# Optimization experiments

Measured on AMD Instinct MI355X. Metric: run time of the kernel, lower is better.

The kernel has to match this reference:

```python
import jax, jax.numpy as jnp
import numpy as np

N, E, L = 20000, 320000, 12
DH, DE, DHE, DRES = 64, 8, 16, 16
SC_F, BB_F = 21, 12
EPS = 1e-5
LETTERS = 'ARNDCQEGHILKMFPSTWYV'
_G = {'A':[0,0,0,0],'R':[1,1,1,1],'N':[1,1,0,0],'D':[1,1,0,0],'C':[1,0,0,0],'Q':[1,1,1,0],'E':[1,1,1,0],'G':[0,0,0,0],'H':[1,1,0,0],'I':[1,1,0,0],'L':[1,1,0,0],'K':[1,1,1,1],'M':[1,1,1,0],'F':[1,1,0,0],'P':[0,0,0,0],'S':[1,0,0,0],'T':[1,0,0,0],'W':[1,1,0,0],'Y':[1,1,0,0],'V':[1,0,0,0]}
CHI_TABLE = jnp.asarray(np.array([_G[a] for a in LETTERS], dtype=np.float32))  # [20,4]


def bn(x, g, b):
    # BatchNorm1d in inference mode with running_mean=0, running_var=1
    return x / jnp.sqrt(1.0 + EPS) * g + b


def gat(x, src, dst, Wl, Wr, att, Wres, bias, edge=None, We=None):
    # single-head GATv2Conv (PyG semantics: messages src->dst, residual projection)
    n = x.shape[0]
    xl = x @ Wl                       # [N,DH]
    m = xl[src] + (x @ Wr)[dst]       # [E,DH] gather
    if edge is not None:
        m = m + edge @ We
    e = jax.nn.leaky_relu(m, 0.2) @ att               # [E]
    emax = jax.ops.segment_max(e, dst, num_segments=n)
    ex = jnp.exp(e - emax[dst])
    den = jax.ops.segment_sum(ex, dst, num_segments=n)
    alpha = ex / (den[dst] + 1e-16)                   # segment softmax over incoming edges
    out = jax.ops.segment_sum(alpha[:, None] * xl[src], dst, num_segments=n)
    return out + bias + x @ Wres


def setup_inputs() -> dict:
    key = jax.random.key(0)
    ks = iter(jax.random.split(key, 80))
    def nrm(*s):
        return jax.random.normal(next(ks), s, jnp.float32) * 0.05
    inp = {}
    inp['sidechain_node_features'] = jax.random.normal(next(ks), (N, SC_F), jnp.float32)
    inp['backbone_node_features'] = jax.random.normal(next(ks), (N, BB_F), jnp.float32)
    inp['sidechain_edge_attrs'] = jax.random.normal(next(ks), (E, DE), jnp.float32)
    inp['sidechain_edges'] = jax.random.randint(next(ks), (2, E), 0, N)
    inp['backbone_edges'] = jax.random.randint(next(ks), (2, E), 0, N)
    inp['residue_ids'] = jax.random.randint(next(ks), (N,), 0, 20)
    inp['sc_emb_W'] = nrm(SC_F, DH); inp['sc_emb_b'] = nrm(DH)
    inp['bb_emb_W'] = nrm(BB_F, DH); inp['bb_emb_b'] = nrm(DH)
    inp['res_table'] = nrm(20, DRES)
    inp['rr_W1'] = nrm(2 * DRES, DHE); inp['rr_b1'] = nrm(DHE)
    inp['rr_W2'] = nrm(DHE, 1); inp['rr_b2'] = nrm(1)
    inp['sc_Wl'] = nrm(L, DH, DH); inp['sc_Wr'] = nrm(L, DH, DH)
    inp['sc_We'] = nrm(L, DE, DH); inp['sc_att'] = nrm(L, DH)
    inp['sc_res'] = nrm(L, DH, DH); inp['sc_bias'] = nrm(L, DH)
    inp['bb_Wl'] = nrm(L, DH, DH); inp['bb_Wr'] = nrm(L, DH, DH)
    inp['bb_att'] = nrm(L, DH); inp['bb_res'] = nrm(L, DH, DH); inp['bb_bias'] = nrm(L, DH)
    inp['eu_W1'] = nrm(L, DE, DHE); inp['eu_b1'] = nrm(L, DHE)
    inp['eu_g'] = jnp.ones((L, DHE)); inp['eu_beta'] = jnp.zeros((L, DHE))
    inp['eu_W2'] = nrm(L, DHE, DE); inp['eu_b2'] = nrm(L, DE)
    inp['bnu_W'] = nrm(DH, DH); inp['bnu_b'] = nrm(DH)
    inp['bnu_g'] = jnp.ones((DH,)); inp['bnu_beta'] = jnp.zeros((DH,))
    inp['af_W'] = nrm(DH, 1); inp['af_b'] = nrm(1)
    inp['af_g'] = jnp.ones((1,)); inp['af_beta'] = jnp.zeros((1,))
    inp['chi_W'] = nrm(4, DH, DH); inp['chi_b'] = nrm(4, DH)
    inp['ad_W1'] = nrm(DH, DH); inp['ad_W2'] = nrm(DH, 1)
    inp['vc_W1'] = nrm(DH, DH); inp['vc_b1'] = nrm(DH)
    inp['vc_W2'] = nrm(DH, 3); inp['vc_b2'] = nrm(3)
    inp['bbh_W1'] = nrm(4, DH, DH); inp['bbh_b1'] = nrm(4, DH)
    inp['phi_W2'] = nrm(DH, 1); inp['psi_W2'] = nrm(DH, 1)
    inp['xca_W2'] = nrm(DH, 3); inp['xca_b2'] = nrm(3)
    inp['vcb_W2'] = nrm(DH, 3); inp['vcb_b2'] = nrm(3)
    return inp


def reference(sidechain_node_features, backbone_node_features, sidechain_edge_attrs, sidechain_edges, backbone_edges, residue_ids, sc_emb_W, sc_emb_b, bb_emb_W, bb_emb_b, res_table, rr_W1, rr_b1, rr_W2, rr_b2, sc_Wl, sc_Wr, sc_We, sc_att, sc_res, sc_bias, bb_Wl, bb_Wr, bb_att, bb_res, bb_bias, eu_W1, eu_b1, eu_g, eu_beta, eu_W2, eu_b2, bnu_W, bnu_b, bnu_g, bnu_beta, af_W, af_b, af_g, af_beta, chi_W, chi_b, ad_W1, ad_W2, vc_W1, vc_b1, vc_W2, vc_b2, bbh_W1, bbh_b1, phi_W2, psi_W2, xca_W2, xca_b2, vcb_W2, vcb_b2):
    # node embeddings (dropout = identity in eval)
    sc = jax.nn.relu(sidechain_node_features @ sc_emb_W + sc_emb_b)
    bb = jax.nn.relu(backbone_node_features @ bb_emb_W + bb_emb_b)
    # residue-relation gating of sidechain edge attrs
    re = res_table[residue_ids]                      # [N,DRES]
    src, dst = sidechain_edges[0], sidechain_edges[1]
    cat = jnp.concatenate([re[src], re[dst]], axis=-1)
    rel = jax.nn.sigmoid(jax.nn.relu(cat @ rr_W1 + rr_b1) @ rr_W2 + rr_b2)  # [E,1]
    ea = sidechain_edge_attrs * rel
    bsrc, bdst = backbone_edges[0], backbone_edges[1]
    for l in range(L):
        # EdgeUpdate: Linear-BN-ReLU-Linear + residual
        h = jax.nn.relu(bn(ea @ eu_W1[l] + eu_b1[l], eu_g[l], eu_beta[l]))
        ea = h @ eu_W2[l] + eu_b2[l] + ea
        sc = gat(sc, src, dst, sc_Wl[l], sc_Wr[l], sc_att[l], sc_res[l], sc_bias[l], ea, sc_We[l])
        bb = gat(bb, bsrc, bdst, bb_Wl[l], bb_Wr[l], bb_att[l], bb_res[l], bb_bias[l])
    # AttentionFusion gates BackboneNodeUpdate(sc) into bb
    sc_up = jax.nn.relu(bn(sc @ bnu_W + bnu_b, bnu_g, bnu_beta))
    attn = jax.nn.sigmoid(bn(sc @ af_W + af_b, af_g, af_beta))
    bb = bb + attn * sc_up
    # sidechain heads with chi masks
    mask = CHI_TABLE[residue_ids]                    # [N,4]
    chis = []
    for i in range(4):
        h = jax.nn.relu(sc @ chi_W[i] + chi_b[i]) * mask[:, i:i + 1]
        chis.append(jax.nn.relu(h @ ad_W1) @ ad_W2)
    v_com = jax.nn.relu(sc @ vc_W1 + vc_b1) @ vc_W2 + vc_b2
    # backbone heads
    phi = jax.nn.relu(bb @ bbh_W1[0] + bbh_b1[0]) @ phi_W2
    psi = jax.nn.relu(bb @ bbh_W1[1] + bbh_b1[1]) @ psi_W2
    X_c_alpha = jax.nn.relu(bb @ bbh_W1[2] + bbh_b1[2]) @ xca_W2 + xca_b2
    V_c_beta = jax.nn.relu(bb @ bbh_W1[3] + bbh_b1[3]) @ vcb_W2 + vcb_b2
    return (chis[0], chis[1], chis[2], chis[3], v_com, phi, psi, X_c_alpha, V_c_beta)
```

## Files before the change

kernel.cpp:

```cpp
#include <hip/hip_runtime.h>
#include <hip/hip_bf16.h>

#define NN 20000
#define NE 320000
#define NL 12
#define BN_C 0.9999950000374997f


#define CHI_PACK ( (0ull<<0)|(4ull<<3)|(2ull<<6)|(2ull<<9)|(1ull<<12)|(3ull<<15)|(3ull<<18)|(0ull<<21) \
                 | (2ull<<24)|(2ull<<27)|(2ull<<30)|(4ull<<33)|(3ull<<36)|(2ull<<39)|(0ull<<42)|(1ull<<45) \
                 | (1ull<<48)|(2ull<<51)|(2ull<<54)|(1ull<<57) )
__device__ __forceinline__ float chi_mask(int res, int i){
  int nchi = (int)((CHI_PACK >> (3*res)) & 7ull);
  return (i < nchi) ? 1.f : 0.f;
}

__device__ __forceinline__ float wsum(float v){
  #pragma unroll
  for (int off = 32; off > 0; off >>= 1) v += __shfl_xor(v, off);
  return v;
}
__device__ __forceinline__ float leaky(float x){
  return fmaxf(x, 0.f) + 0.2f*fminf(x, 0.f);
}

__global__ __launch_bounds__(256) void k_init(int* p, int n){
  int i = blockIdx.x*256 + threadIdx.x;
  if (i < n) p[i] = 0;
}

__global__ __launch_bounds__(256) void k_mark(float* out){
  int i = blockIdx.x*256 + threadIdx.x;
  if (i < NN) out[i] = 9.0f;
}

__global__ __launch_bounds__(256) void k_pre(
    const float* __restrict__ Xsc, const float* __restrict__ Xbb,
    const float* __restrict__ Wsc, const float* __restrict__ bsc,
    const float* __restrict__ Wbb, const float* __restrict__ bbb,
    const int* __restrict__ scE, const int* __restrict__ bbE,
    float* __restrict__ sc, float* __restrict__ bbuf, int* cnt_sc, int* cnt_bb){
  int b = blockIdx.x, t = threadIdx.x;
  if (b < 5000){
    int tid = b*256 + t;
    int node = tid >> 6, d = tid & 63;
    float acc = bsc[d];
    #pragma unroll
    for (int k = 0; k < 21; k++) acc += Xsc[node*21+k] * Wsc[k*64+d];
    sc[tid] = fmaxf(acc, 0.f);
  } else if (b < 10000){
    int tid = (b-5000)*256 + t;
    int node = tid >> 6, d = tid & 63;
    float acc = bbb[d];
    #pragma unroll
    for (int k = 0; k < 12; k++) acc += Xbb[node*12+k] * Wbb[k*64+d];
    bbuf[tid] = fmaxf(acc, 0.f);
  } else if (b < 11250){
    int e = (b-10000)*256 + t;
    atomicAdd(&cnt_sc[scE[NE + e]], 1);
  } else {
    int e = (b-11250)*256 + t;
    atomicAdd(&cnt_bb[bbE[NE + e]], 1);
  }
}

__global__ __launch_bounds__(256) void k_scan(
    int* cnt_sc, int* cnt_bb, int* rp_sc, int* rp_bb,
    const float* __restrict__ resT, const float* __restrict__ rrW1,
    const float* __restrict__ rrb1, const float* __restrict__ rrW2,
    const float* __restrict__ rrb2, float* relTab){
  int t = threadIdx.x;
  if (blockIdx.x == 2){
    __shared__ float sRT[320], sW1[512], sB1[16], sW2[16];
    for (int i = t; i < 320; i += 256) sRT[i] = resT[i];
    for (int i = t; i < 512; i += 256) sW1[i] = rrW1[i];
    if (t < 16){ sB1[t] = rrb1[t]; sW2[t] = rrW2[t]; }
    __syncthreads();
    float b2v = rrb2[0];
    for (int p = t; p < 400; p += 256){
      int a = p / 20, c = p % 20;
      const float* ra = &sRT[a*16];
      const float* rc = &sRT[c*16];
      float z = b2v;
      #pragma unroll
      for (int j = 0; j < 16; j++){
        float h = sB1[j];
        #pragma unroll
        for (int i = 0; i < 16; i++) h += ra[i] * sW1[i*16+j];
        #pragma unroll
        for (int i = 0; i < 16; i++) h += rc[i] * sW1[(16+i)*16+j];
        z += fmaxf(h, 0.f) * sW2[j];
      }
      relTab[p] = 1.f / (1.f + __expf(-z));
    }
    return;
  }
  int* cnt = blockIdx.x ? cnt_bb : cnt_sc;
  int* rp  = blockIdx.x ? rp_bb  : rp_sc;
  __shared__ int s[256];
  const int CH = 79;
  int beg = t * CH;
  int sum = 0;
  for (int i = beg; i < beg + CH && i < NN; i++) sum += cnt[i];
  s[t] = sum; __syncthreads();
  for (int off = 1; off < 256; off <<= 1){
    int v = (t >= off) ? s[t-off] : 0;
    __syncthreads();
    s[t] += v;
    __syncthreads();
  }
  int run = (t == 0) ? 0 : s[t-1];
  for (int i = beg; i < beg + CH && i < NN; i++){
    int c = cnt[i];
    rp[i] = run;
    cnt[i] = run;
    run += c;
  }
  if (t == 0) rp[NN] = NE;
}

__global__ __launch_bounds__(256) void k_scatter(
    const int* __restrict__ scE, const int* __restrict__ bbE, const int* __restrict__ rid,
    const float* __restrict__ relTab, const float* __restrict__ attrs,
    int* cur_sc, int* cur_bb, int* __restrict__ ps_sc, int* __restrict__ ps_bb,
    float* __restrict__ ea){
  int b = blockIdx.x, t = threadIdx.x;
  if (b < 1250){
    int e = b*256 + t;
    int s = scE[e], d = scE[NE + e];
    float rel = relTab[rid[s]*20 + rid[d]];
    float4 A = ((const float4*)attrs)[e*2];
    float4 B = ((const float4*)attrs)[e*2+1];
    A.x *= rel; A.y *= rel; A.z *= rel; A.w *= rel;
    B.x *= rel; B.y *= rel; B.z *= rel; B.w *= rel;
    int pos = atomicAdd(&cur_sc[d], 1);
    ps_sc[pos] = s;
    ((float4*)ea)[pos*2]   = A;
    ((float4*)ea)[pos*2+1] = B;
  } else {
    int e = (b-1250)*256 + t;
    int s = bbE[e], d = bbE[NE + e];
    int pos = atomicAdd(&cur_bb[d], 1);
    ps_bb[pos] = s;
  }
}

__device__ void node_mm(float* sx, const float* __restrict__ x,
                        const float* __restrict__ Wl, const float* __restrict__ Wr,
                        const float* __restrict__ Wres, const float* __restrict__ bias, int l,
                        float* __restrict__ xl, float* __restrict__ xr, float* __restrict__ base,
                        int tile){
  int t = threadIdx.x;
  for (int i = t; i < 1024; i += 256) sx[i] = x[tile*1024 + i];
  __syncthreads();
  int d = t & 63, r = t >> 6;
  int wo = l*4096 + d;
  float aL[4] = {0,0,0,0}, aR[4] = {0,0,0,0}, aB[4];
  float bv = bias[l*64 + d];
  #pragma unroll
  for (int j = 0; j < 4; j++) aB[j] = bv;
  #pragma unroll 4
  for (int k = 0; k < 64; k++){
    float wl = Wl[wo + k*64], wr = Wr[wo + k*64], ws = Wres[wo + k*64];
    #pragma unroll
    for (int j = 0; j < 4; j++){
      float xv = sx[(r + 4*j)*64 + k];
      aL[j] += xv*wl; aR[j] += xv*wr; aB[j] += xv*ws;
    }
  }
  int n0 = tile*16 + r;
  #pragma unroll
  for (int j = 0; j < 4; j++){
    int n = n0 + 4*j;
    xl[n*64+d] = aL[j]; xr[n*64+d] = aR[j]; base[n*64+d] = aB[j];
  }
}

__global__ __launch_bounds__(256) void k_layer1(
    float* __restrict__ ea, int l,
    const float* __restrict__ euW1, const float* __restrict__ eub1,
    const float* __restrict__ eug, const float* __restrict__ eube,
    const float* __restrict__ euW2, const float* __restrict__ eub2,
    const float* __restrict__ sc, const float* __restrict__ bbv,
    const float* __restrict__ scWl, const float* __restrict__ scWr,
    const float* __restrict__ scRes, const float* __restrict__ scBias,
    const float* __restrict__ bbWl, const float* __restrict__ bbWr,
    const float* __restrict__ bbRes, const float* __restrict__ bbBias,
    float* __restrict__ xl_sc, float* __restrict__ xr_sc, float* __restrict__ bs_sc,
    float* __restrict__ xl_bb, float* __restrict__ xr_bb, float* __restrict__ bs_bb){
  __shared__ float smem[1024];
  int b = blockIdx.x, t = threadIdx.x;
  if (b < 1250){
    float* sW1 = smem;        float* sB1 = smem+128; float* sG  = smem+144;
    float* sBe = smem+160;    float* sW2 = smem+176; float* sB2 = smem+304;
    for (int i = t; i < 128; i += 256){ sW1[i] = euW1[l*128+i]; sW2[i] = euW2[l*128+i]; }
    if (t < 16){ sB1[t] = eub1[l*16+t]; sG[t] = eug[l*16+t]; sBe[t] = eube[l*16+t]; }
    if (t < 8) sB2[t] = eub2[l*8+t];
    __syncthreads();
    int e = b*256 + t;
    float4 A = ((const float4*)ea)[e*2];
    float4 B = ((const float4*)ea)[e*2+1];
    float a[8] = {A.x,A.y,A.z,A.w,B.x,B.y,B.z,B.w};
    float h[16];
    #pragma unroll
    for (int j = 0; j < 16; j++){
      float v = sB1[j];
      #pragma unroll
      for (int i = 0; i < 8; i++) v += a[i] * sW1[i*16+j];
      h[j] = fmaxf(v*BN_C*sG[j] + sBe[j], 0.f);
    }
    #pragma unroll
    for (int i = 0; i < 8; i++){
      float v = sB2[i] + a[i];
      #pragma unroll
      for (int j = 0; j < 16; j++) v += h[j] * sW2[j*8+i];
      a[i] = v;
    }
    ((float4*)ea)[e*2]   = make_float4(a[0],a[1],a[2],a[3]);
    ((float4*)ea)[e*2+1] = make_float4(a[4],a[5],a[6],a[7]);
  } else if (b < 2500){
    node_mm(smem, sc, scWl, scWr, scRes, scBias, l, xl_sc, xr_sc, bs_sc, b-1250);
  } else {
    node_mm(smem, bbv, bbWl, bbWr, bbRes, bbBias, l, xl_bb, xr_bb, bs_bb, b-2500);
  }
}

__global__ __launch_bounds__(256) void k_agg(
    float* __restrict__ sc, float* __restrict__ bbv, int l,
    const float* __restrict__ xl_sc, const float* __restrict__ xr_sc, const float* __restrict__ bs_sc,
    const float* __restrict__ xl_bb, const float* __restrict__ xr_bb, const float* __restrict__ bs_bb,
    const int* __restrict__ rp_sc, const int* __restrict__ ps_sc,
    const int* __restrict__ rp_bb, const int* __restrict__ ps_bb,
    const float* __restrict__ ea, const float* __restrict__ We,
    const float* __restrict__ scAtt, const float* __restrict__ bbAtt){
  int b = blockIdx.x;
  int lane = threadIdx.x & 63, wid = threadIdx.x >> 6;
  int half = lane >> 5, l2 = lane & 31;
  bool is_sc = b < 5000;
  int n = (is_sc ? b : b - 5000)*4 + wid;
  const float* xl = is_sc ? xl_sc : xl_bb;
  const float* xr = is_sc ? xr_sc : xr_bb;
  const float* bs = is_sc ? bs_sc : bs_bb;
  const int* rp = is_sc ? rp_sc : rp_bb;
  const int* ps = is_sc ? ps_sc : ps_bb;
  const float2* xl2 = (const float2*)xl;
  float2 att2 = ((const float2*)((is_sc ? scAtt : bbAtt) + l*64))[l2];
  float2 w[8];
  if (is_sc){
    #pragma unroll
    for (int j = 0; j < 8; j++) w[j] = ((const float2*)(We + l*512 + j*64))[l2];
  }
  int beg = rp[n], end = rp[n+1];
  float2 xr2 = ((const float2*)xr)[n*32 + l2];
  float ox = 0.f, oy = 0.f, s = 0.f;
  if (beg < end){
    int last = end - 1;
    int ia = min(beg + half, last);
    int ib = min(beg + 2 + half, last);
    float2 vA = xl2[ps[ia]*32 + l2];
    float2 vB = xl2[ps[ib]*32 + l2];
    for (int eid = beg; eid < end; eid += 4){
      int nx = eid + 4;
      int ia_n = min(nx + half, last);
      int ib_n = min(nx + 2 + half, last);
      float2 vA_n = xl2[ps[ia_n]*32 + l2];
      float2 vB_n = xl2[ps[ib_n]*32 + l2];
      bool va = eid + half < end;
      bool vb = eid + 2 + half < end;
      float mAx = vA.x + xr2.x, mAy = vA.y + xr2.y;
      float mBx = vB.x + xr2.x, mBy = vB.y + xr2.y;
      if (is_sc){
        int cia = min(eid + half, last);
        int cib = min(eid + 2 + half, last);
        const float4* pa4 = (const float4*)(ea + (size_t)cia*8);
        float4 A = pa4[0], B = pa4[1];
        float av[8] = {A.x,A.y,A.z,A.w,B.x,B.y,B.z,B.w};
        #pragma unroll
        for (int j = 0; j < 8; j++){ mAx += av[j]*w[j].x; mAy += av[j]*w[j].y; }
        const float4* pb4 = (const float4*)(ea + (size_t)cib*8);
        A = pb4[0]; B = pb4[1];
        float bvv[8] = {A.x,A.y,A.z,A.w,B.x,B.y,B.z,B.w};
        #pragma unroll
        for (int j = 0; j < 8; j++){ mBx += bvv[j]*w[j].x; mBy += bvv[j]*w[j].y; }
      }
      float eA = leaky(mAx)*att2.x + leaky(mAy)*att2.y;
      float eB = leaky(mBx)*att2.x + leaky(mBy)*att2.y;
      #pragma unroll
      for (int off = 1; off <= 16; off <<= 1){
        eA += __shfl_xor(eA, off);
        eB += __shfl_xor(eB, off);
      }
      float pA = va ? __expf(eA) : 0.f;
      float pB = vb ? __expf(eB) : 0.f;
      ox += pA*vA.x + pB*vB.x;
      oy += pA*vA.y + pB*vB.y;
      s  += pA + pB;
      vA = vA_n; vB = vB_n;
    }
  }
  ox += __shfl_xor(ox, 32);
  oy += __shfl_xor(oy, 32);
  s  += __shfl_xor(s, 32);
  if (half == 0){
    float2 bsv = ((const float2*)bs)[n*32 + l2];
    float inv = 1.f/(s + 1e-16f);
    float2 r;
    r.x = ox*inv + bsv.x;
    r.y = oy*inv + bsv.y;
    ((float2*)(is_sc ? sc : bbv))[n*32 + l2] = r;
  }
}

__global__ __launch_bounds__(256) void k_heads(
    const float* __restrict__ sc, const float* __restrict__ bbv, const int* __restrict__ rid,
    const float* __restrict__ bnuW, const float* __restrict__ bnub,
    const float* __restrict__ bnug, const float* __restrict__ bnube,
    const float* __restrict__ afW, const float* __restrict__ afb,
    const float* __restrict__ afg, const float* __restrict__ afbe,
    const float* __restrict__ vcW1, const float* __restrict__ vcb1,
    const float* __restrict__ vcW2, const float* __restrict__ vcb2,
    const float* __restrict__ chiW, const float* __restrict__ chib,
    const float* __restrict__ adW1, const float* __restrict__ adW2,
    const float* __restrict__ bbhW1, const float* __restrict__ bbhb1,
    const float* __restrict__ phiW2, const float* __restrict__ psiW2,
    const float* __restrict__ xcaW2, const float* __restrict__ xcab2,
    const float* __restrict__ vcbW2, const float* __restrict__ vcbb2,
    float* __restrict__ out){
  __shared__ float sx[1024];
  __shared__ float sh[1024];
  __shared__ int srid[16];
  int b = blockIdx.x, t = threadIdx.x;
  int d = t & 63, r = t >> 6;
  if (b < 1250){
    int tile = b;
    for (int i = t; i < 1024; i += 256) sx[i] = sc[tile*1024 + i];
    if (t < 16) srid[t] = rid[tile*16 + t];
    __syncthreads();
    for (int i = 0; i < 4; i++){
      const float* W = chiW + i*4096;
      float acc[4] = {0,0,0,0};
      #pragma unroll 4
      for (int k = 0; k < 64; k++){
        float w = W[k*64+d];
        #pragma unroll
        for (int j = 0; j < 4; j++) acc[j] += sx[(r + 4*j)*64 + k] * w;
      }
      float bi = chib[i*64+d];
      #pragma unroll
      for (int j = 0; j < 4; j++){
        float mk = chi_mask(srid[r + 4*j], i);
        sh[(r + 4*j)*64 + d] = fmaxf(acc[j] + bi, 0.f) * mk;
      }
      __syncthreads();
      float a2[4] = {0,0,0,0};
      #pragma unroll 4
      for (int k = 0; k < 64; k++){
        float w = adW1[k*64+d];
        #pragma unroll
        for (int j = 0; j < 4; j++) a2[j] += sh[(r + 4*j)*64 + k] * w;
      }
      float w2 = adW2[d];
      #pragma unroll
      for (int j = 0; j < 4; j++){
        float p = wsum(fmaxf(a2[j], 0.f) * w2);
        if (d == 0) out[i*NN + tile*16 + r + 4*j] = p;
      }
      __syncthreads();
    }
  } else {
    int tile = b - 1250;
    for (int i = t; i < 1024; i += 256){ sx[i] = sc[tile*1024 + i]; sh[i] = bbv[tile*1024 + i]; }
    __syncthreads();
    float aU[4] = {0,0,0,0}, aV[4] = {0,0,0,0};
    #pragma unroll 4
    for (int k = 0; k < 64; k++){
      float wu = bnuW[k*64+d], wv = vcW1[k*64+d];
      #pragma unroll
      for (int j = 0; j < 4; j++){
        float xv = sx[(r + 4*j)*64 + k];
        aU[j] += xv*wu; aV[j] += xv*wv;
      }
    }
    float afwd = afW[d];
    float bnubd = bnub[d], bnugd = bnug[d], bnubed = bnube[d];
    float vcb1d = vcb1[d];
    float afbv = afb[0], afgv = afg[0], afbev = afbe[0];
    #pragma unroll
    for (int j = 0; j < 4; j++){
      int node = tile*16 + r + 4*j;
      float z = wsum(sx[(r + 4*j)*64 + d] * afwd);
      float attn = 1.f / (1.f + __expf(-((z + afbv)*BN_C*afgv + afbev)));
      float u = fmaxf((aU[j] + bnubd)*BN_C*bnugd + bnubed, 0.f);
      sh[(r + 4*j)*64 + d] += attn*u;
      float vh = fmaxf(aV[j] + vcb1d, 0.f);
      #pragma unroll
      for (int c = 0; c < 3; c++){
        float p = wsum(vh * vcW2[d*3+c]);
        if (d == 0) out[4*NN + node*3 + c] = p + vcb2[c];
      }
    }
    __syncthreads();
    for (int i = 0; i < 4; i++){
      const float* W = bbhW1 + i*4096;
      float acc[4] = {0,0,0,0};
      #pragma unroll 4
      for (int k = 0; k < 64; k++){
        float w = W[k*64+d];
        #pragma unroll
        for (int j = 0; j < 4; j++) acc[j] += sh[(r + 4*j)*64 + k] * w;
      }
      float bi = bbhb1[i*64+d];
      if (i < 2){
        float w2 = (i == 0) ? phiW2[d] : psiW2[d];
        #pragma unroll
        for (int j = 0; j < 4; j++){
          float p = wsum(fmaxf(acc[j] + bi, 0.f) * w2);
          if (d == 0) out[(7+i)*NN + tile*16 + r + 4*j] = p;
        }
      } else {
        const float* W2 = (i == 2) ? xcaW2 : vcbW2;
        const float* B2 = (i == 2) ? xcab2 : vcbb2;
        int off = (i == 2) ? 9*NN : 12*NN;
        #pragma unroll
        for (int j = 0; j < 4; j++){
          float h = fmaxf(acc[j] + bi, 0.f);
          #pragma unroll
          for (int c = 0; c < 3; c++){
            float p = wsum(h * W2[d*3+c]);
            if (d == 0) out[off + (tile*16 + r + 4*j)*3 + c] = p + B2[c];
          }
        }
      }
    }
  }
}

extern "C" __attribute__((visibility("default")))
void kernel_launch(void* const* d_in, const int* in_sizes, int n_in,
                   void* d_out, int out_size, void* d_ws, size_t ws_size,
                   hipStream_t stream) {
  (void)hipGetLastError();

  const float* Xsc   = (const float*)d_in[0];
  const float* Xbb   = (const float*)d_in[1];
  const float* attrs = (const float*)d_in[2];
  const int*  scE   = (const int*)d_in[3];
  const int*  bbE   = (const int*)d_in[4];
  const int*  rid   = (const int*)d_in[5];
  const float* scembW=(const float*)d_in[6];  const float* scembb=(const float*)d_in[7];
  const float* bbembW=(const float*)d_in[8];  const float* bbembb=(const float*)d_in[9];
  const float* resT  =(const float*)d_in[10];
  const float* rrW1  =(const float*)d_in[11]; const float* rrb1  =(const float*)d_in[12];
  const float* rrW2  =(const float*)d_in[13]; const float* rrb2  =(const float*)d_in[14];
  const float* scWl  =(const float*)d_in[15]; const float* scWr  =(const float*)d_in[16];
  const float* scWe  =(const float*)d_in[17]; const float* scAtt =(const float*)d_in[18];
  const float* scRes =(const float*)d_in[19]; const float* scBias=(const float*)d_in[20];
  const float* bbWl  =(const float*)d_in[21]; const float* bbWr  =(const float*)d_in[22];
  const float* bbAtt =(const float*)d_in[23]; const float* bbRes =(const float*)d_in[24];
  const float* bbBias=(const float*)d_in[25];
  const float* euW1  =(const float*)d_in[26]; const float* eub1  =(const float*)d_in[27];
  const float* eug   =(const float*)d_in[28]; const float* eube  =(const float*)d_in[29];
  const float* euW2  =(const float*)d_in[30]; const float* eub2  =(const float*)d_in[31];
  const float* bnuW  =(const float*)d_in[32]; const float* bnub  =(const float*)d_in[33];
  const float* bnug  =(const float*)d_in[34]; const float* bnube =(const float*)d_in[35];
  const float* afW   =(const float*)d_in[36]; const float* afb   =(const float*)d_in[37];
  const float* afg   =(const float*)d_in[38]; const float* afbe  =(const float*)d_in[39];
  const float* chiW  =(const float*)d_in[40]; const float* chib  =(const float*)d_in[41];
  const float* adW1  =(const float*)d_in[42]; const float* adW2  =(const float*)d_in[43];
  const float* vcW1  =(const float*)d_in[44]; const float* vcb1  =(const float*)d_in[45];
  const float* vcW2  =(const float*)d_in[46]; const float* vcb2  =(const float*)d_in[47];
  const float* bbhW1 =(const float*)d_in[48]; const float* bbhb1 =(const float*)d_in[49];
  const float* phiW2 =(const float*)d_in[50]; const float* psiW2 =(const float*)d_in[51];
  const float* xcaW2 =(const float*)d_in[52]; const float* xcab2 =(const float*)d_in[53];
  const float* vcbW2 =(const float*)d_in[54]; const float* vcbb2 =(const float*)d_in[55];
  float* out = (float*)d_out;

  size_t need = 1024 + (size_t)(8*NN*64 + NE*8)*4 + (size_t)(2*(NN+1) + 2*NN + 2*NE)*4;
  if (ws_size < need){
    k_mark<<<(NN+255)/256, 256, 0, stream>>>(out);
    return;
  }
  float* relTab = (float*)d_ws;
  float* f = (float*)((char*)d_ws + 1024);
  float* sc    = f; f += NN*64;
  float* bbuf  = f; f += NN*64;
  float* xl_sc = f; f += NN*64;
  float* xr_sc = f; f += NN*64;
  float* bs_sc = f; f += NN*64;
  float* xl_bb = f; f += NN*64;
  float* xr_bb = f; f += NN*64;
  float* bs_bb = f; f += NN*64;
  float* ea    = f; f += NE*8;
  int* ip = (int*)f;
  int* rp_sc  = ip; ip += NN+1;
  int* rp_bb  = ip; ip += NN+1;
  int* cnt_sc = ip; ip += NN;
  int* cnt_bb = ip; ip += NN;
  int* ps_sc  = ip; ip += NE;
  int* ps_bb  = ip; ip += NE;

  k_init<<<(2*NN + 255)/256, 256, 0, stream>>>(cnt_sc, 2*NN);
  k_pre<<<12500, 256, 0, stream>>>(Xsc, Xbb, scembW, scembb, bbembW, bbembb,
                                   scE, bbE, sc, bbuf, cnt_sc, cnt_bb);
  k_scan<<<3, 256, 0, stream>>>(cnt_sc, cnt_bb, rp_sc, rp_bb,
                                resT, rrW1, rrb1, rrW2, rrb2, relTab);
  k_scatter<<<2500, 256, 0, stream>>>(scE, bbE, rid, relTab, attrs,
                                      cnt_sc, cnt_bb, ps_sc, ps_bb, ea);
  for (int l = 0; l < NL; l++){
    k_layer1<<<3750, 256, 0, stream>>>(ea, l,
        euW1, eub1, eug, eube, euW2, eub2,
        sc, bbuf,
        scWl, scWr, scRes, scBias,
        bbWl, bbWr, bbRes, bbBias,
        xl_sc, xr_sc, bs_sc, xl_bb, xr_bb, bs_bb);
    k_agg<<<10000, 256, 0, stream>>>(sc, bbuf, l,
        xl_sc, xr_sc, bs_sc, xl_bb, xr_bb, bs_bb,
        rp_sc, ps_sc, rp_bb, ps_bb,
        ea, scWe, scAtt, bbAtt);
  }
  k_heads<<<2500, 256, 0, stream>>>(sc, bbuf, rid,
      bnuW, bnub, bnug, bnube, afW, afb, afg, afbe,
      vcW1, vcb1, vcW2, vcb2,
      chiW, chib, adW1, adW2, bbhW1, bbhb1,
      phiW2, psiW2, xcaW2, xcab2, vcbW2, vcbb2, out);
}
```

Baseline: 1.343 ms.

## Enlarge node matmul tiles, interleave agg blocks across XCDs, use nontemporal loads

The node projection in k_layer1 now computes 32 nodes per block instead of 16. This reuses each weight load across twice as many rows and halves the node-block count (3750 to 2500 blocks). k_agg remaps block indices so sidechain and backbone work is interleaved across the 8 XCDs, which aims at better L2 locality and load balance. Edge index and edge-attribute streams in k_agg use nontemporal loads to avoid polluting cache needed for gathered xl rows. Costs are more registers and shared memory per block and fewer blocks for latency hiding.

```diff
diff --git a/kernel.cpp b/kernel.cpp
--- a/kernel.cpp
+++ b/kernel.cpp
@@ -14,6 +14,10 @@
   int nchi = (int)((CHI_PACK >> (3*res)) & 7ull);
   return (i < nchi) ? 1.f : 0.f;
 }
+
+typedef float vf4 __attribute__((ext_vector_type(4)));
+__device__ __forceinline__ vf4 ldnt4(const float* p){ return __builtin_nontemporal_load((const vf4*)p); }
+__device__ __forceinline__ int  ldnti(const int* p){ return __builtin_nontemporal_load(p); }
 
 __device__ __forceinline__ float wsum(float v){
   #pragma unroll
@@ -145,37 +149,6 @@
   }
 }
 
-__device__ void node_mm(float* sx, const float* __restrict__ x,
-                        const float* __restrict__ Wl, const float* __restrict__ Wr,
-                        const float* __restrict__ Wres, const float* __restrict__ bias, int l,
-                        float* __restrict__ xl, float* __restrict__ xr, float* __restrict__ base,
-                        int tile){
-  int t = threadIdx.x;
-  for (int i = t; i < 1024; i += 256) sx[i] = x[tile*1024 + i];
-  __syncthreads();
-  int d = t & 63, r = t >> 6;
-  int wo = l*4096 + d;
-  float aL[4] = {0,0,0,0}, aR[4] = {0,0,0,0}, aB[4];
-  float bv = bias[l*64 + d];
-  #pragma unroll
-  for (int j = 0; j < 4; j++) aB[j] = bv;
-  #pragma unroll 4
-  for (int k = 0; k < 64; k++){
-    float wl = Wl[wo + k*64], wr = Wr[wo + k*64], ws = Wres[wo + k*64];
-    #pragma unroll
-    for (int j = 0; j < 4; j++){
-      float xv = sx[(r + 4*j)*64 + k];
-      aL[j] += xv*wl; aR[j] += xv*wr; aB[j] += xv*ws;
-    }
-  }
-  int n0 = tile*16 + r;
-  #pragma unroll
-  for (int j = 0; j < 4; j++){
-    int n = n0 + 4*j;
-    xl[n*64+d] = aL[j]; xr[n*64+d] = aR[j]; base[n*64+d] = aB[j];
-  }
-}
-
 __global__ __launch_bounds__(256) void k_layer1(
     float* __restrict__ ea, int l,
     const float* __restrict__ euW1, const float* __restrict__ eub1,
@@ -188,7 +161,7 @@
     const float* __restrict__ bbRes, const float* __restrict__ bbBias,
     float* __restrict__ xl_sc, float* __restrict__ xr_sc, float* __restrict__ bs_sc,
     float* __restrict__ xl_bb, float* __restrict__ xr_bb, float* __restrict__ bs_bb){
-  __shared__ float smem[1024];
+  __shared__ float smem[2048];
   int b = blockIdx.x, t = threadIdx.x;
   if (b < 1250){
     float* sW1 = smem;        float* sB1 = smem+128; float* sG  = smem+144;
@@ -218,10 +191,40 @@
     }
     ((float4*)ea)[e*2]   = make_float4(a[0],a[1],a[2],a[3]);
     ((float4*)ea)[e*2+1] = make_float4(a[4],a[5],a[6],a[7]);
-  } else if (b < 2500){
-    node_mm(smem, sc, scWl, scWr, scRes, scBias, l, xl_sc, xr_sc, bs_sc, b-1250);
   } else {
-    node_mm(smem, bbv, bbWl, bbWr, bbRes, bbBias, l, xl_bb, xr_bb, bs_bb, b-2500);
+    bool is_sc = b < 1875;
+    int tile = is_sc ? (b-1250) : (b-1875);
+    const float* x  = is_sc ? sc : bbv;
+    const float* Wl = is_sc ? scWl : bbWl;
+    const float* Wr = is_sc ? scWr : bbWr;
+    const float* Ws = is_sc ? scRes : bbRes;
+    const float* bias = is_sc ? scBias : bbBias;
+    float* xl = is_sc ? xl_sc : xl_bb;
+    float* xr = is_sc ? xr_sc : xr_bb;
+    float* bs = is_sc ? bs_sc : bs_bb;
+    for (int i = t; i < 2048; i += 256) smem[i] = x[tile*2048 + i];
+    __syncthreads();
+    int d = t & 63, r = t >> 6;
+    int wo = l*4096 + d;
+    float aL[8] = {0,0,0,0,0,0,0,0}, aR[8] = {0,0,0,0,0,0,0,0}, aB[8];
+    float bv = bias[l*64 + d];
+    #pragma unroll
+    for (int j = 0; j < 8; j++) aB[j] = bv;
+    #pragma unroll 2
+    for (int k = 0; k < 64; k++){
+      float wl = Wl[wo + k*64], wr = Wr[wo + k*64], ws = Ws[wo + k*64];
+      #pragma unroll
+      for (int j = 0; j < 8; j++){
+        float xv = smem[(r + 4*j)*64 + k];
+        aL[j] += xv*wl; aR[j] += xv*wr; aB[j] += xv*ws;
+      }
+    }
+    int n0 = tile*32 + r;
+    #pragma unroll
+    for (int j = 0; j < 8; j++){
+      int n = n0 + 4*j;
+      xl[n*64+d] = aL[j]; xr[n*64+d] = aR[j]; bs[n*64+d] = aB[j];
+    }
   }
 }
 
@@ -233,11 +236,12 @@
     const int* __restrict__ rp_bb, const int* __restrict__ ps_bb,
     const float* __restrict__ ea, const float* __restrict__ We,
     const float* __restrict__ scAtt, const float* __restrict__ bbAtt){
-  int b = blockIdx.x;
+  int x = blockIdx.x;
   int lane = threadIdx.x & 63, wid = threadIdx.x >> 6;
   int half = lane >> 5, l2 = lane & 31;
-  bool is_sc = b < 5000;
-  int n = (is_sc ? b : b - 5000)*4 + wid;
+  int xcd = x & 7;
+  bool is_sc = xcd < 4;
+  int n = ((x >> 3)*4 + (xcd & 3))*4 + wid;
   const float* xl = is_sc ? xl_sc : xl_bb;
   const float* xr = is_sc ? xr_sc : xr_bb;
   const float* bs = is_sc ? bs_sc : bs_bb;
@@ -257,14 +261,14 @@
     int last = end - 1;
     int ia = min(beg + half, last);
     int ib = min(beg + 2 + half, last);
-    float2 vA = xl2[ps[ia]*32 + l2];
-    float2 vB = xl2[ps[ib]*32 + l2];
+    float2 vA = xl2[ldnti(ps + ia)*32 + l2];
+    float2 vB = xl2[ldnti(ps + ib)*32 + l2];
     for (int eid = beg; eid < end; eid += 4){
       int nx = eid + 4;
       int ia_n = min(nx + half, last);
       int ib_n = min(nx + 2 + half, last);
-      float2 vA_n = xl2[ps[ia_n]*32 + l2];
-      float2 vB_n = xl2[ps[ib_n]*32 + l2];
+      float2 vA_n = xl2[ldnti(ps + ia_n)*32 + l2];
+      float2 vB_n = xl2[ldnti(ps + ib_n)*32 + l2];
       bool va = eid + half < end;
       bool vb = eid + 2 + half < end;
       float mAx = vA.x + xr2.x, mAy = vA.y + xr2.y;
@@ -272,13 +276,13 @@
       if (is_sc){
         int cia = min(eid + half, last);
         int cib = min(eid + 2 + half, last);
-        const float4* pa4 = (const float4*)(ea + (size_t)cia*8);
-        float4 A = pa4[0], B = pa4[1];
+        vf4 A = ldnt4(ea + (size_t)cia*8);
+        vf4 B = ldnt4(ea + (size_t)cia*8 + 4);
         float av[8] = {A.x,A.y,A.z,A.w,B.x,B.y,B.z,B.w};
         #pragma unroll
         for (int j = 0; j < 8; j++){ mAx += av[j]*w[j].x; mAy += av[j]*w[j].y; }
-        const float4* pb4 = (const float4*)(ea + (size_t)cib*8);
-        A = pb4[0]; B = pb4[1];
+        A = ldnt4(ea + (size_t)cib*8);
+        B = ldnt4(ea + (size_t)cib*8 + 4);
         float bvv[8] = {A.x,A.y,A.z,A.w,B.x,B.y,B.z,B.w};
         #pragma unroll
         for (int j = 0; j < 8; j++){ mBx += bvv[j]*w[j].x; mBy += bvv[j]*w[j].y; }
@@ -507,7 +511,7 @@
   k_scatter<<<2500, 256, 0, stream>>>(scE, bbE, rid, relTab, attrs,
                                       cnt_sc, cnt_bb, ps_sc, ps_bb, ea);
   for (int l = 0; l < NL; l++){
-    k_layer1<<<3750, 256, 0, stream>>>(ea, l,
+    k_layer1<<<2500, 256, 0, stream>>>(ea, l,
         euW1, eub1, eug, eube, euW2, eub2,
         sc, bbuf,
         scWl, scWr, scRes, scBias,
```

Measured after the change: 1.708 ms. 1.27x slower.
